# Performance work log

Measured on AMD Instinct MI355X. Metric: run time of the kernel, lower is better.

The kernel has to match this reference:

```python
import jax, jax.numpy as jnp
import numpy as np

VOCAB = 32000
ROUTE_BIAS = 10.0  # weight on the deterministic one-hot route vs mu logits


def setup_inputs() -> dict:
    key = jax.random.key(0)
    k1, k2, k3, k4, k5, k6 = jax.random.split(key, 6)
    B, S, H = 2, 4096, 1024
    E, Ie = 8, 512  # intermediate_size=4096 -> expert_intermediate=512, fused dim=2*Ie=1024
    return {
        "hidden_states": jax.random.normal(k1, (B, S, H), dtype=jnp.float32),
        "token_ids": jax.random.randint(k2, (B, S), 0, VOCAB),
        "mu": jax.random.normal(k3, (B, S, H), dtype=jnp.float32),
        "gate_up_proj": jax.random.normal(k4, (E, H, 2 * Ie), dtype=jnp.float32) * 0.02,
        "down_proj": jax.random.normal(k5, (E, Ie, H), dtype=jnp.float32) * 0.02,
        "mu_router_w": jax.random.normal(k6, (E, H), dtype=jnp.float32) * 0.02,
    }


def reference(hidden_states, token_ids, mu, gate_up_proj, down_proj, mu_router_w):
    B, S, H = hidden_states.shape
    E, _, F2 = gate_up_proj.shape
    Ie = F2 // 2
    N = B * S

    # deterministic token->expert routing, optionally perturbed by mu logits
    token_to_expert = jnp.arange(VOCAB, dtype=jnp.int32) % E
    base_expert = token_to_expert[jnp.clip(token_ids, 0, VOCAB - 1)]      # [B,S]
    mu_logits = jnp.einsum('bsh,eh->bse', mu, mu_router_w)                 # [B,S,E]
    combined = jax.nn.one_hot(base_expert, E, dtype=mu_logits.dtype) * ROUTE_BIAS + mu_logits
    expert_ids = jnp.argmax(combined, axis=-1).reshape(N)                  # [N]

    x = hidden_states.reshape(N, H)
    tok = jnp.arange(N)

    # compute per-expert GEMM then select per-token expert output
    # (same math as gathering the full weight slab per token, without the
    #  N*H*2Ie gathered-weight blowup of the original torch code)
    gu_all = jnp.einsum('nh,ehf->enf', x, gate_up_proj)                    # [E,N,2Ie]
    gu = gu_all[expert_ids, tok]                                           # [N,2Ie]
    gate, up = gu[:, :Ie], gu[:, Ie:]
    inter = jax.nn.silu(gate) * up                                         # [N,Ie]

    z_all = jnp.einsum('ni,eih->enh', inter, down_proj)                    # [E,N,H]
    out = z_all[expert_ids, tok].reshape(B, S, H)
    return out
```

## Files before the change

kernel.cpp:

```cpp
#include <hip/hip_runtime.h>
#include <hip/hip_bf16.h>
#include <stdint.h>

typedef __bf16 bf16x8 __attribute__((ext_vector_type(8)));
typedef float f32x4 __attribute__((ext_vector_type(4)));

#define ROUTE_BIAS_F 10.0f
#define VOCAB_SZ 32000

__device__ __forceinline__ unsigned short f2bf(float f) {
    union { float f; unsigned u; } v; v.f = f;
    unsigned u = v.u;
    unsigned r = u + 0x7FFFu + ((u >> 16) & 1u);
    return (unsigned short)(r >> 16);
}
__device__ __forceinline__ float bf2f(unsigned short s) {
    union { unsigned u; float f; } v; v.u = ((unsigned)s) << 16;
    return v.f;
}
__device__ __forceinline__ void ld16(const unsigned short* g, unsigned short* l) {
    __builtin_amdgcn_global_load_lds(
        (const __attribute__((address_space(1))) void*)g,
        (__attribute__((address_space(3))) void*)l, 16, 0, 0);
}

__global__ void k_prep(const float* __restrict__ hidden, const float* __restrict__ mu,
                       const int* __restrict__ tok_ids, const float* __restrict__ rw,
                       unsigned short* __restrict__ xb, int* __restrict__ eids,
                       int H, int N) {
    int lane = threadIdx.x & 63;
    int wv   = threadIdx.x >> 6;
    int tok  = blockIdx.x * 4 + wv;
    if (tok >= N) return;
    const float4* hp = (const float4*)(hidden + (size_t)tok * H);
    const float4* mp = (const float4*)(mu + (size_t)tok * H);
    const float4* rp = (const float4*)rw;
    ushort4* xp = (ushort4*)(xb + (size_t)tok * H);
    int H4 = H >> 2;
    float acc[8];
#pragma unroll
    for (int e = 0; e < 8; ++e) acc[e] = 0.f;
#pragma unroll
    for (int j = 0; j < 4; ++j) {
        int idx = lane + 64 * j;
        float4 h4 = hp[idx];
        ushort4 o;
        o.x = f2bf(h4.x); o.y = f2bf(h4.y); o.z = f2bf(h4.z); o.w = f2bf(h4.w);
        xp[idx] = o;
        float4 m4 = mp[idx];
#pragma unroll
        for (int e = 0; e < 8; ++e) {
            float4 w4 = rp[e * H4 + idx];
            acc[e] += m4.x * w4.x + m4.y * w4.y + m4.z * w4.z + m4.w * w4.w;
        }
    }
#pragma unroll
    for (int e = 0; e < 8; ++e) {
        float v = acc[e];
#pragma unroll
        for (int off = 32; off > 0; off >>= 1) v += __shfl_xor(v, off);
        acc[e] = v;
    }
    if (lane == 0) {
        int t = tok_ids[tok];
        if (t < 0) t = 0;
        if (t > VOCAB_SZ - 1) t = VOCAB_SZ - 1;
        int be = t % 8;
        float best = -1e30f; int bi = 0;
#pragma unroll
        for (int e = 0; e < 8; ++e) {
            float v = acc[e] + (e == be ? ROUTE_BIAS_F : 0.f);
            if (v > best) { best = v; bi = e; }
        }
        eids[tok] = bi;
    }
}

__global__ __launch_bounds__(256) void k_transpose_all(
        const float* __restrict__ gup, const float* __restrict__ dnp,
        unsigned short* __restrict__ wgut, unsigned short* __restrict__ wdnt,
        int H, int F2, int Ie) {
    __shared__ float tile[64][65];
    int z = blockIdx.z;
    const float* inp; unsigned short* outp; int R, C;
    if (z < 8) { R = H; C = F2; inp = gup + (size_t)z * R * C;       outp = wgut + (size_t)z * R * C; }
    else       { R = Ie; C = H; inp = dnp + (size_t)(z - 8) * R * C; outp = wdnt + (size_t)(z - 8) * R * C; }
    int c0 = blockIdx.x * 64, r0 = blockIdx.y * 64;
    if (r0 >= R) return;
    int tid = threadIdx.x;
    int tr = tid >> 4;
    int tc = (tid & 15) * 4;
#pragma unroll
    for (int p = 0; p < 4; ++p) {
        float4 v = *(const float4*)&inp[(size_t)(r0 + tr + 16 * p) * C + c0 + tc];
        tile[tr + 16 * p][tc + 0] = v.x;
        tile[tr + 16 * p][tc + 1] = v.y;
        tile[tr + 16 * p][tc + 2] = v.z;
        tile[tr + 16 * p][tc + 3] = v.w;
    }
    __syncthreads();
#pragma unroll
    for (int p = 0; p < 4; ++p) {
        int c = tr + 16 * p;
        ushort4 o;
        o.x = f2bf(tile[tc + 0][c]);
        o.y = f2bf(tile[tc + 1][c]);
        o.z = f2bf(tile[tc + 2][c]);
        o.w = f2bf(tile[tc + 3][c]);
        *(ushort4*)&outp[(size_t)(c0 + c) * R + r0 + tc] = o;
    }
}

__global__ void k_count(const int* __restrict__ eids,
                        int* __restrict__ blockcnt, int N) {
    __shared__ int cnt[8];
    int tid = threadIdx.x;
    if (tid < 8) cnt[tid] = 0;
    __syncthreads();
    int tok = blockIdx.x * 256 + tid;
    int lane = tid & 63;
    int eid = (tok < N) ? eids[tok] : -1;
#pragma unroll
    for (int e = 0; e < 8; ++e) {
        unsigned long long m = __ballot(eid == e);
        if (lane == 0 && m) atomicAdd(&cnt[e], __popcll(m));
    }
    __syncthreads();
    if (tid < 8) blockcnt[blockIdx.x * 8 + tid] = cnt[tid];
}

__global__ void k_scan(const int* __restrict__ blockcnt,
                       int* __restrict__ counts, int* __restrict__ base_,
                       int* __restrict__ offs, int NB) {
    __shared__ int tot[8];
    int lane = threadIdx.x;
    int e = lane >> 3, g = lane & 7;
    int v[4];
    int s = 0;
#pragma unroll
    for (int i = 0; i < 4; ++i) { v[i] = s; s += blockcnt[(g * 4 + i) * 8 + e]; }
    int inc = s;
#pragma unroll
    for (int d = 1; d < 8; d <<= 1) {
        int t = __shfl_up(inc, d);
        if (g >= d) inc += t;
    }
    int excl = inc - s;
#pragma unroll
    for (int i = 0; i < 4; ++i) offs[(g * 4 + i) * 8 + e] = excl + v[i];
    if (g == 7) { counts[e] = inc; tot[e] = inc; }
    __syncthreads();
    if (lane == 0) {
        int s2 = 0;
#pragma unroll
        for (int i = 0; i < 8; ++i) { base_[i] = s2; s2 += tot[i]; }
    }
}

__global__ void k_scatter(const int* __restrict__ eids,
                          const int* __restrict__ offs,
                          int* __restrict__ list, int N) {
    __shared__ int wavecnt[4][8];
    int tid = threadIdx.x;
    int lane = tid & 63, wv = tid >> 6;
    int tok = blockIdx.x * 256 + tid;
    int eid = (tok < N) ? eids[tok] : -1;
    unsigned long long below = (1ull << lane) - 1ull;
    int myrank = 0;
#pragma unroll
    for (int e = 0; e < 8; ++e) {
        unsigned long long m = __ballot(eid == e);
        if (lane == 0) wavecnt[wv][e] = __popcll(m);
        if (eid == e) myrank = __popcll(m & below);
    }
    __syncthreads();
    if (eid >= 0) {
        int pre = 0;
        for (int w = 0; w < wv; ++w) pre += wavecnt[w][eid];
        int pos = offs[blockIdx.x * 8 + eid] + pre + myrank;
        list[eid * N + pos] = tok;
    }
}

#define TM 128
#define TN 128
#define TK 64

__global__ __launch_bounds__(256, 2) void k_gemm_gateup(
    const unsigned short* __restrict__ X,
    const unsigned short* __restrict__ Wt,
    unsigned short* __restrict__ IT,
    const int* __restrict__ counts, const int* __restrict__ base_,
    const int* __restrict__ list, int N, int H, int Ie) {
    int bid = blockIdx.x;
    int e = bid & 7;
    int t = bid >> 3;
    int nt = t & 7;
    int mt = t >> 3;
    int cnt = counts[e];
    int m0 = mt * TM;
    if (m0 >= cnt) return;
    int F2 = 2 * Ie;

    __shared__ __align__(16) unsigned short As[2][TM * TK];
    __shared__ __align__(16) unsigned short Bs[2][TN * TK];

    int tid = threadIdx.x;
    int lane = tid & 63, wv = tid >> 6;
    int wr = (wv >> 1) * 64;
    int wc = (wv & 1) * 64;

    int rowg = lane >> 3;
    int sl   = (lane & 7) ^ rowg;

    const unsigned short* ag[4];
    const unsigned short* bg[4];
#pragma unroll
    for (int i = 0; i < 4; ++i) {
        int r = wv * 32 + i * 8 + rowg;
        int gr = m0 + r;
        int tokrow = (gr < cnt) ? list[e * N + gr] : 0;
        ag[i] = X + (size_t)tokrow * H + sl * 8;
    }
#pragma unroll
    for (int i = 0; i < 4; ++i) {
        int r = wv * 32 + i * 8 + rowg;
        int wrow = (r & 1) * Ie + nt * 64 + (r >> 1);
        bg[i] = Wt + ((size_t)e * F2 + wrow) * H + sl * 8;
    }

    f32x4 acc[4][4];
#pragma unroll
    for (int i = 0; i < 4; ++i)
#pragma unroll
        for (int j = 0; j < 4; ++j) acc[i][j] = (f32x4)(0.f);

    int q = lane >> 4, m = lane & 15;
    int sw = m & 7;

    int nk = H / TK;
#pragma unroll
    for (int i = 0; i < 4; ++i) ld16(ag[i], &As[0][(wv * 32 + i * 8) * TK]);
#pragma unroll
    for (int i = 0; i < 4; ++i) ld16(bg[i], &Bs[0][(wv * 32 + i * 8) * TK]);
    __syncthreads();

    int cur = 0;
    for (int t_ = 0; t_ < nk; ++t_) {
        if (t_ + 1 < nk) {
            int k1 = (t_ + 1) * TK;
#pragma unroll
            for (int i = 0; i < 4; ++i) ld16(ag[i] + k1, &As[cur ^ 1][(wv * 32 + i * 8) * TK]);
#pragma unroll
            for (int i = 0; i < 4; ++i) ld16(bg[i] + k1, &Bs[cur ^ 1][(wv * 32 + i * 8) * TK]);
        }
        const unsigned short* Ac = As[cur];
        const unsigned short* Bc = Bs[cur];
#pragma unroll
        for (int ks = 0; ks < TK; ks += 32) {
            int kc = ks >> 3;
            int ck = ((kc + q) ^ sw) << 3;
            bf16x8 af[4], bfr[4];
#pragma unroll
            for (int im = 0; im < 4; ++im)
                af[im] = *(const bf16x8*)&Ac[(wr + m + im * 16) * TK + ck];
#pragma unroll
            for (int in_ = 0; in_ < 4; ++in_)
                bfr[in_] = *(const bf16x8*)&Bc[(wc + m + in_ * 16) * TK + ck];
#pragma unroll
            for (int im = 0; im < 4; ++im)
#pragma unroll
                for (int in_ = 0; in_ < 4; ++in_)
                    acc[im][in_] = __builtin_amdgcn_mfma_f32_16x16x32_bf16(
                        af[im], bfr[in_], acc[im][in_], 0, 0, 0);
        }
        __syncthreads();
        cur ^= 1;
    }

    int b = base_[e];
    int nt64 = nt * 64;
#pragma unroll
    for (int im = 0; im < 4; ++im) {
#pragma unroll
        for (int j = 0; j < 4; ++j) {
            int row = wr + im * 16 + q * 4 + j;
            int gr = m0 + row;
#pragma unroll
            for (int in_ = 0; in_ < 4; ++in_) {
                float v = acc[im][in_][j];
                float u = __shfl_xor(v, 1);
                float g = v;
                float s = g / (1.f + __expf(-g));
                float res = s * u;
                if (!(lane & 1) && gr < cnt) {
                    int oc = nt64 + ((wc + in_ * 16 + m) >> 1);
                    IT[(size_t)(b + gr) * Ie + oc] = f2bf(res);
                }
            }
        }
    }
}

__global__ __launch_bounds__(256, 2) void k_gemm_down(
    const unsigned short* __restrict__ IT,
    const unsigned short* __restrict__ Wt,
    float* __restrict__ OUT,
    const int* __restrict__ counts, const int* __restrict__ base_,
    const int* __restrict__ list, int N, int Ie, int H) {
    int bid = blockIdx.x;
    int e = bid & 7;
    int t = bid >> 3;
    int nt = t & 7;
    int mt = t >> 3;
    int cnt = counts[e];
    int m0 = mt * TM;
    if (m0 >= cnt) return;
    int n0 = nt * TN;
    int b = base_[e];

    __shared__ __align__(16) unsigned short As[2][TM * TK];
    __shared__ __align__(16) unsigned short Bs[2][TN * TK];

    int tid = threadIdx.x;
    int lane = tid & 63, wv = tid >> 6;
    int wr = (wv >> 1) * 64;
    int wc = (wv & 1) * 64;

    int rowg = lane >> 3;
    int sl   = (lane & 7) ^ rowg;

    const unsigned short* We = Wt + ((size_t)e * H + n0) * Ie;
    const unsigned short* ag[4];
    const unsigned short* bg[4];
#pragma unroll
    for (int i = 0; i < 4; ++i) {
        int r = wv * 32 + i * 8 + rowg;
        int gr = m0 + r;
        int arow = (gr < cnt) ? (b + gr) : b;
        ag[i] = IT + (size_t)arow * Ie + sl * 8;
    }
#pragma unroll
    for (int i = 0; i < 4; ++i) {
        int r = wv * 32 + i * 8 + rowg;
        bg[i] = We + (size_t)r * Ie + sl * 8;
    }

    f32x4 acc[4][4];
#pragma unroll
    for (int i = 0; i < 4; ++i)
#pragma unroll
        for (int j = 0; j < 4; ++j) acc[i][j] = (f32x4)(0.f);

    int q = lane >> 4, m = lane & 15;
    int sw = m & 7;

    int nk = Ie / TK;
#pragma unroll
    for (int i = 0; i < 4; ++i) ld16(ag[i], &As[0][(wv * 32 + i * 8) * TK]);
#pragma unroll
    for (int i = 0; i < 4; ++i) ld16(bg[i], &Bs[0][(wv * 32 + i * 8) * TK]);
    __syncthreads();

    int cur = 0;
    for (int t_ = 0; t_ < nk; ++t_) {
        if (t_ + 1 < nk) {
            int k1 = (t_ + 1) * TK;
#pragma unroll
            for (int i = 0; i < 4; ++i) ld16(ag[i] + k1, &As[cur ^ 1][(wv * 32 + i * 8) * TK]);
#pragma unroll
            for (int i = 0; i < 4; ++i) ld16(bg[i] + k1, &Bs[cur ^ 1][(wv * 32 + i * 8) * TK]);
        }
        const unsigned short* Ac = As[cur];
        const unsigned short* Bc = Bs[cur];
#pragma unroll
        for (int ks = 0; ks < TK; ks += 32) {
            int kc = ks >> 3;
            int ck = ((kc + q) ^ sw) << 3;
            bf16x8 af[4], bfr[4];
#pragma unroll
            for (int im = 0; im < 4; ++im)
                af[im] = *(const bf16x8*)&Ac[(wr + m + im * 16) * TK + ck];
#pragma unroll
            for (int in_ = 0; in_ < 4; ++in_)
                bfr[in_] = *(const bf16x8*)&Bc[(wc + m + in_ * 16) * TK + ck];
#pragma unroll
            for (int im = 0; im < 4; ++im)
#pragma unroll
                for (int in_ = 0; in_ < 4; ++in_)
                    acc[im][in_] = __builtin_amdgcn_mfma_f32_16x16x32_bf16(
                        af[im], bfr[in_], acc[im][in_], 0, 0, 0);
        }
        __syncthreads();
        cur ^= 1;
    }

#pragma unroll
    for (int im = 0; im < 4; ++im) {
#pragma unroll
        for (int j = 0; j < 4; ++j) {
            int row = wr + im * 16 + q * 4 + j;
            int gr = m0 + row;
            if (gr < cnt) {
                int tok = list[e * N + gr];
                float* orow = OUT + (size_t)tok * H + n0;
#pragma unroll
                for (int in_ = 0; in_ < 4; ++in_) {
                    int col = wc + in_ * 16 + m;
                    orow[col] = acc[im][in_][j];
                }
            }
        }
    }
}

extern "C" void kernel_launch(void* const* d_in, const int* in_sizes, int n_in,
                              void* d_out, int out_size, void* d_ws, size_t ws_size,
                              hipStream_t stream) {
    const float* hidden   = (const float*)d_in[0];
    const int*   tok_ids  = (const int*)d_in[1];
    const float* mu       = (const float*)d_in[2];
    const float* gup      = (const float*)d_in[3];
    const float* dnp      = (const float*)d_in[4];
    const float* rw       = (const float*)d_in[5];
    float* out = (float*)d_out;

    int N  = in_sizes[1];
    int H  = in_sizes[0] / N;
    int E  = in_sizes[5] / H;
    int F2 = in_sizes[3] / (E * H);
    int Ie = F2 / 2;

    int NB = (N + 255) / 256;

    char* ws = (char*)d_ws;
    size_t o = 0;
    auto alloc = [&](size_t sz) {
        size_t r = o;
        o += (sz + 255) & ~(size_t)255;
        return r;
    };
    int* counts   = (int*)(ws + alloc((size_t)E * 4));
    int* base_    = (int*)(ws + alloc((size_t)E * 4));
    int* eids     = (int*)(ws + alloc((size_t)N * 4));
    int* blockcnt = (int*)(ws + alloc((size_t)NB * 8 * 4));
    int* offs     = (int*)(ws + alloc((size_t)NB * 8 * 4));
    int* list     = (int*)(ws + alloc((size_t)E * N * 4));
    unsigned short* xb   = (unsigned short*)(ws + alloc((size_t)N * H * 2));
    unsigned short* wgut = (unsigned short*)(ws + alloc((size_t)E * F2 * H * 2));
    unsigned short* wdnt = (unsigned short*)(ws + alloc((size_t)E * H * Ie * 2));
    unsigned short* it   = (unsigned short*)(ws + alloc((size_t)N * Ie * 2));

    k_prep<<<dim3((N + 3) / 4), dim3(256), 0, stream>>>(hidden, mu, tok_ids, rw, xb, eids, H, N);

    k_transpose_all<<<dim3(16, 16, 16), dim3(256), 0, stream>>>(gup, dnp, wgut, wdnt, H, F2, Ie);

    k_count<<<dim3(NB), dim3(256), 0, stream>>>(eids, blockcnt, N);
    k_scan<<<dim3(1), dim3(64), 0, stream>>>(blockcnt, counts, base_, offs, NB);
    k_scatter<<<dim3(NB), dim3(256), 0, stream>>>(eids, offs, list, N);

    int MT = (N + TM - 1) / TM;
    k_gemm_gateup<<<dim3(E * MT * (Ie / 64)), dim3(256), 0, stream>>>(
        xb, wgut, it, counts, base_, list, N, H, Ie);

    k_gemm_down<<<dim3(E * MT * (H / TN)), dim3(256), 0, stream>>>(
        it, wdnt, out, counts, base_, list, N, Ie, H);
}
```

Before: 239.4 us.

## Use persistent grid-stride M-tiles in MoE GEMMs; single-buffer down GEMM for occupancy

Both expert GEMMs now launch a fixed grid of 8 slots per expert and N-tile, and each block loops over M-tiles with stride 8. Previously the grid was sized for the worst case of N/128 M-tiles per expert, and most blocks exited early. The down GEMM drops LDS double buffering so three blocks can share a CU, and the gate-up MFMA loop raises wave priority with s_setprio. The down GEMM no longer overlaps loads with compute, and the fixed 8 slots may leave CUs idle when expert counts are uneven.

New measurement: 239.1 us. About the same (-0.1%).

```diff
diff --git a/kernel.cpp b/kernel.cpp
--- a/kernel.cpp
+++ b/kernel.cpp
@@ -196,11 +196,11 @@
     int e = bid & 7;
     int t = bid >> 3;
     int nt = t & 7;
-    int mt = t >> 3;
+    int slot = t >> 3;
     int cnt = counts[e];
-    int m0 = mt * TM;
-    if (m0 >= cnt) return;
     int F2 = 2 * Ie;
+    int b = base_[e];
+    int nt64 = nt * 64;
 
     __shared__ __align__(16) unsigned short As[2][TM * TK];
     __shared__ __align__(16) unsigned short Bs[2][TN * TK];
@@ -213,96 +213,101 @@
     int rowg = lane >> 3;
     int sl   = (lane & 7) ^ rowg;
 
-    const unsigned short* ag[4];
     const unsigned short* bg[4];
 #pragma unroll
     for (int i = 0; i < 4; ++i) {
         int r = wv * 32 + i * 8 + rowg;
-        int gr = m0 + r;
-        int tokrow = (gr < cnt) ? list[e * N + gr] : 0;
-        ag[i] = X + (size_t)tokrow * H + sl * 8;
-    }
-#pragma unroll
-    for (int i = 0; i < 4; ++i) {
-        int r = wv * 32 + i * 8 + rowg;
-        int wrow = (r & 1) * Ie + nt * 64 + (r >> 1);
+        int wrow = (r & 1) * Ie + nt64 + (r >> 1);
         bg[i] = Wt + ((size_t)e * F2 + wrow) * H + sl * 8;
     }
-
-    f32x4 acc[4][4];
-#pragma unroll
-    for (int i = 0; i < 4; ++i)
-#pragma unroll
-        for (int j = 0; j < 4; ++j) acc[i][j] = (f32x4)(0.f);
 
     int q = lane >> 4, m = lane & 15;
     int sw = m & 7;
-
     int nk = H / TK;
-#pragma unroll
-    for (int i = 0; i < 4; ++i) ld16(ag[i], &As[0][(wv * 32 + i * 8) * TK]);
-#pragma unroll
-    for (int i = 0; i < 4; ++i) ld16(bg[i], &Bs[0][(wv * 32 + i * 8) * TK]);
-    __syncthreads();
-
-    int cur = 0;
-    for (int t_ = 0; t_ < nk; ++t_) {
-        if (t_ + 1 < nk) {
-            int k1 = (t_ + 1) * TK;
-#pragma unroll
-            for (int i = 0; i < 4; ++i) ld16(ag[i] + k1, &As[cur ^ 1][(wv * 32 + i * 8) * TK]);
-#pragma unroll
-            for (int i = 0; i < 4; ++i) ld16(bg[i] + k1, &Bs[cur ^ 1][(wv * 32 + i * 8) * TK]);
-        }
-        const unsigned short* Ac = As[cur];
-        const unsigned short* Bc = Bs[cur];
-#pragma unroll
-        for (int ks = 0; ks < TK; ks += 32) {
-            int kc = ks >> 3;
-            int ck = ((kc + q) ^ sw) << 3;
-            bf16x8 af[4], bfr[4];
-#pragma unroll
-            for (int im = 0; im < 4; ++im)
-                af[im] = *(const bf16x8*)&Ac[(wr + m + im * 16) * TK + ck];
-#pragma unroll
-            for (int in_ = 0; in_ < 4; ++in_)
-                bfr[in_] = *(const bf16x8*)&Bc[(wc + m + in_ * 16) * TK + ck];
-#pragma unroll
-            for (int im = 0; im < 4; ++im)
+
+    for (int mt = slot; mt * TM < cnt; mt += 8) {
+        int m0 = mt * TM;
+
+        const unsigned short* ag[4];
+#pragma unroll
+        for (int i = 0; i < 4; ++i) {
+            int r = wv * 32 + i * 8 + rowg;
+            int gr = m0 + r;
+            int tokrow = (gr < cnt) ? list[e * N + gr] : 0;
+            ag[i] = X + (size_t)tokrow * H + sl * 8;
+        }
+
+        f32x4 acc[4][4];
+#pragma unroll
+        for (int i = 0; i < 4; ++i)
+#pragma unroll
+            for (int j = 0; j < 4; ++j) acc[i][j] = (f32x4)(0.f);
+
+#pragma unroll
+        for (int i = 0; i < 4; ++i) ld16(ag[i], &As[0][(wv * 32 + i * 8) * TK]);
+#pragma unroll
+        for (int i = 0; i < 4; ++i) ld16(bg[i], &Bs[0][(wv * 32 + i * 8) * TK]);
+        __syncthreads();
+
+        int cur = 0;
+        for (int t_ = 0; t_ < nk; ++t_) {
+            if (t_ + 1 < nk) {
+                int k1 = (t_ + 1) * TK;
+#pragma unroll
+                for (int i = 0; i < 4; ++i) ld16(ag[i] + k1, &As[cur ^ 1][(wv * 32 + i * 8) * TK]);
+#pragma unroll
+                for (int i = 0; i < 4; ++i) ld16(bg[i] + k1, &Bs[cur ^ 1][(wv * 32 + i * 8) * TK]);
+            }
+            const unsigned short* Ac = As[cur];
+            const unsigned short* Bc = Bs[cur];
+            __builtin_amdgcn_s_setprio(1);
+#pragma unroll
+            for (int ks = 0; ks < TK; ks += 32) {
+                int kc = ks >> 3;
+                int ck = ((kc + q) ^ sw) << 3;
+                bf16x8 af[4], bfr[4];
+#pragma unroll
+                for (int im = 0; im < 4; ++im)
+                    af[im] = *(const bf16x8*)&Ac[(wr + m + im * 16) * TK + ck];
 #pragma unroll
                 for (int in_ = 0; in_ < 4; ++in_)
-                    acc[im][in_] = __builtin_amdgcn_mfma_f32_16x16x32_bf16(
-                        af[im], bfr[in_], acc[im][in_], 0, 0, 0);
-        }
-        __syncthreads();
-        cur ^= 1;
-    }
-
-    int b = base_[e];
-    int nt64 = nt * 64;
-#pragma unroll
-    for (int im = 0; im < 4; ++im) {
-#pragma unroll
-        for (int j = 0; j < 4; ++j) {
-            int row = wr + im * 16 + q * 4 + j;
-            int gr = m0 + row;
-#pragma unroll
-            for (int in_ = 0; in_ < 4; ++in_) {
-                float v = acc[im][in_][j];
-                float u = __shfl_xor(v, 1);
-                float g = v;
-                float s = g / (1.f + __expf(-g));
-                float res = s * u;
-                if (!(lane & 1) && gr < cnt) {
-                    int oc = nt64 + ((wc + in_ * 16 + m) >> 1);
-                    IT[(size_t)(b + gr) * Ie + oc] = f2bf(res);
+                    bfr[in_] = *(const bf16x8*)&Bc[(wc + m + in_ * 16) * TK + ck];
+#pragma unroll
+                for (int im = 0; im < 4; ++im)
+#pragma unroll
+                    for (int in_ = 0; in_ < 4; ++in_)
+                        acc[im][in_] = __builtin_amdgcn_mfma_f32_16x16x32_bf16(
+                            af[im], bfr[in_], acc[im][in_], 0, 0, 0);
+            }
+            __builtin_amdgcn_s_setprio(0);
+            __syncthreads();
+            cur ^= 1;
+        }
+
+#pragma unroll
+        for (int im = 0; im < 4; ++im) {
+#pragma unroll
+            for (int j = 0; j < 4; ++j) {
+                int row = wr + im * 16 + q * 4 + j;
+                int gr = m0 + row;
+#pragma unroll
+                for (int in_ = 0; in_ < 4; ++in_) {
+                    float v = acc[im][in_][j];
+                    float u = __shfl_xor(v, 1);
+                    float g = v;
+                    float s = g / (1.f + __expf(-g));
+                    float res = s * u;
+                    if (!(lane & 1) && gr < cnt) {
+                        int oc = nt64 + ((wc + in_ * 16 + m) >> 1);
+                        IT[(size_t)(b + gr) * Ie + oc] = f2bf(res);
+                    }
                 }
             }
         }
     }
 }
 
-__global__ __launch_bounds__(256, 2) void k_gemm_down(
+__global__ __launch_bounds__(256, 3) void k_gemm_down(
     const unsigned short* __restrict__ IT,
     const unsigned short* __restrict__ Wt,
     float* __restrict__ OUT,
@@ -312,15 +317,13 @@
     int e = bid & 7;
     int t = bid >> 3;
     int nt = t & 7;
-    int mt = t >> 3;
+    int slot = t >> 3;
     int cnt = counts[e];
-    int m0 = mt * TM;
-    if (m0 >= cnt) return;
     int n0 = nt * TN;
     int b = base_[e];
 
-    __shared__ __align__(16) unsigned short As[2][TM * TK];
-    __shared__ __align__(16) unsigned short Bs[2][TN * TK];
+    __shared__ __align__(16) unsigned short As[TM * TK];
+    __shared__ __align__(16) unsigned short Bs[TN * TK];
 
     int tid = threadIdx.x;
     int lane = tid & 63, wv = tid >> 6;
@@ -331,83 +334,77 @@
     int sl   = (lane & 7) ^ rowg;
 
     const unsigned short* We = Wt + ((size_t)e * H + n0) * Ie;
-    const unsigned short* ag[4];
     const unsigned short* bg[4];
-#pragma unroll
-    for (int i = 0; i < 4; ++i) {
-        int r = wv * 32 + i * 8 + rowg;
-        int gr = m0 + r;
-        int arow = (gr < cnt) ? (b + gr) : b;
-        ag[i] = IT + (size_t)arow * Ie + sl * 8;
-    }
 #pragma unroll
     for (int i = 0; i < 4; ++i) {
         int r = wv * 32 + i * 8 + rowg;
         bg[i] = We + (size_t)r * Ie + sl * 8;
     }
 
-    f32x4 acc[4][4];
-#pragma unroll
-    for (int i = 0; i < 4; ++i)
-#pragma unroll
-        for (int j = 0; j < 4; ++j) acc[i][j] = (f32x4)(0.f);
-
     int q = lane >> 4, m = lane & 15;
     int sw = m & 7;
 
-    int nk = Ie / TK;
-#pragma unroll
-    for (int i = 0; i < 4; ++i) ld16(ag[i], &As[0][(wv * 32 + i * 8) * TK]);
-#pragma unroll
-    for (int i = 0; i < 4; ++i) ld16(bg[i], &Bs[0][(wv * 32 + i * 8) * TK]);
-    __syncthreads();
-
-    int cur = 0;
-    for (int t_ = 0; t_ < nk; ++t_) {
-        if (t_ + 1 < nk) {
-            int k1 = (t_ + 1) * TK;
-#pragma unroll
-            for (int i = 0; i < 4; ++i) ld16(ag[i] + k1, &As[cur ^ 1][(wv * 32 + i * 8) * TK]);
-#pragma unroll
-            for (int i = 0; i < 4; ++i) ld16(bg[i] + k1, &Bs[cur ^ 1][(wv * 32 + i * 8) * TK]);
-        }
-        const unsigned short* Ac = As[cur];
-        const unsigned short* Bc = Bs[cur];
-#pragma unroll
-        for (int ks = 0; ks < TK; ks += 32) {
-            int kc = ks >> 3;
-            int ck = ((kc + q) ^ sw) << 3;
-            bf16x8 af[4], bfr[4];
-#pragma unroll
-            for (int im = 0; im < 4; ++im)
-                af[im] = *(const bf16x8*)&Ac[(wr + m + im * 16) * TK + ck];
-#pragma unroll
-            for (int in_ = 0; in_ < 4; ++in_)
-                bfr[in_] = *(const bf16x8*)&Bc[(wc + m + in_ * 16) * TK + ck];
-#pragma unroll
-            for (int im = 0; im < 4; ++im)
+    for (int mt = slot; mt * TM < cnt; mt += 8) {
+        int m0 = mt * TM;
+
+        const unsigned short* ag[4];
+#pragma unroll
+        for (int i = 0; i < 4; ++i) {
+            int r = wv * 32 + i * 8 + rowg;
+            int gr = m0 + r;
+            int arow = (gr < cnt) ? (b + gr) : b;
+            ag[i] = IT + (size_t)arow * Ie + sl * 8;
+        }
+
+        f32x4 acc[4][4];
+#pragma unroll
+        for (int i = 0; i < 4; ++i)
+#pragma unroll
+            for (int j = 0; j < 4; ++j) acc[i][j] = (f32x4)(0.f);
+
+        for (int k0 = 0; k0 < Ie; k0 += TK) {
+#pragma unroll
+            for (int i = 0; i < 4; ++i)
+                ld16(ag[i] + k0, &As[(wv * 32 + i * 8) * TK]);
+#pragma unroll
+            for (int i = 0; i < 4; ++i)
+                ld16(bg[i] + k0, &Bs[(wv * 32 + i * 8) * TK]);
+            __syncthreads();
+#pragma unroll
+            for (int ks = 0; ks < TK; ks += 32) {
+                int kc = ks >> 3;
+                int ck = ((kc + q) ^ sw) << 3;
+                bf16x8 af[4], bfr[4];
+#pragma unroll
+                for (int im = 0; im < 4; ++im)
+                    af[im] = *(const bf16x8*)&As[(wr + m + im * 16) * TK + ck];
 #pragma unroll
                 for (int in_ = 0; in_ < 4; ++in_)
-                    acc[im][in_] = __builtin_amdgcn_mfma_f32_16x16x32_bf16(
-                        af[im], bfr[in_], acc[im][in_], 0, 0, 0);
-        }
-        __syncthreads();
-        cur ^= 1;
-    }
-
-#pragma unroll
-    for (int im = 0; im < 4; ++im) {
-#pragma unroll
-        for (int j = 0; j < 4; ++j) {
-            int row = wr + im * 16 + q * 4 + j;
-            int gr = m0 + row;
-            if (gr < cnt) {
-                int tok = list[e * N + gr];
-                float* orow = OUT + (size_t)tok * H + n0;
-#pragma unroll
-                for (int in_ = 0; in_ < 4; ++in_) {
-                    int col = wc + in_ * 16 + m;
-                    orow[col] = acc[im][in_][j];
+                    bfr[in_] = *(const bf16x8*)&Bs[(wc + m + in_ * 16) * TK + ck];
+#pragma unroll
+                for (int im = 0; im < 4; ++im)
+#pragma unroll
+                    for (int in_ = 0; in_ < 4; ++in_)
+                        acc[im][in_] = __builtin_amdgcn_mfma_f32_16x16x32_bf16(
+                            af[im], bfr[in_], acc[im][in_], 0, 0, 0);
+            }
+            __syncthreads();
+        }
+
+#pragma unroll
+        for (int im = 0; im < 4; ++im) {
+#pragma unroll
+            for (int j = 0; j < 4; ++j) {
+                int row = wr + im * 16 + q * 4 + j;
+                int gr = m0 + row;
+                if (gr < cnt) {
+                    int tok = list[e * N + gr];
+                    float* orow = OUT + (size_t)tok * H + n0;
+#pragma unroll
+                    for (int in_ = 0; in_ < 4; ++in_) {
+                        int col = wc + in_ * 16 + m;
+                        orow[col] = acc[im][in_][j];
+                    }
                 }
             }
         }
@@ -459,10 +456,9 @@
     k_scan<<<dim3(1), dim3(64), 0, stream>>>(blockcnt, counts, base_, offs, NB);
     k_scatter<<<dim3(NB), dim3(256), 0, stream>>>(eids, offs, list, N);
 
-    int MT = (N + TM - 1) / TM;
-    k_gemm_gateup<<<dim3(E * MT * (Ie / 64)), dim3(256), 0, stream>>>(
+    k_gemm_gateup<<<dim3(E * (Ie / 64) * 8), dim3(256), 0, stream>>>(
         xb, wgut, it, counts, base_, list, N, H, Ie);
 
-    k_gemm_down<<<dim3(E * MT * (H / TN)), dim3(256), 0, stream>>>(
+    k_gemm_down<<<dim3(E * (H / TN) * 8), dim3(256), 0, stream>>>(
         it, wdnt, out, counts, base_, list, N, Ie, H);
 }
```
